# Performance work log

Hardware: AMD Instinct MI355X
Metric: run time of the kernel (lower is better)

## Reference

```python
import jax, jax.numpy as jnp
import numpy as np

B, K, N = 32768, 8, 64
TN = 3 * N


def _P():
    # 9x9 vec-transpose permutation (matches the hand-built P in the torch module)
    P = np.zeros((9, 9), dtype=np.float32)
    rows = [0, 1, 2, 3, 4, 5, 6, 7, 8]
    cols = [0, 3, 6, 1, 4, 7, 2, 5, 8]
    P[rows, cols] = 1.0
    return jnp.asarray(P)


def _precompute(b, w, lam):
    # b: (K,3,N), w: (1,N,1), lam: scalar
    wsum = jnp.sum(w)
    b_w = (b @ w)[..., 0] / wsum                       # (K,3)
    sw = jnp.sqrt(w).reshape(1, 1, N)                  # (1,1,N)
    bar_b = sw * (b - b_w[:, :, None])                 # (K,3,N)
    bar_B = bar_b.transpose(0, 2, 1).reshape(K, TN).T  # (3N,K)
    bar_H = 2.0 * (bar_B.T @ bar_B + lam * jnp.eye(K, dtype=b.dtype))
    Hinv = jnp.linalg.inv(bar_H)
    Htemp = Hinv @ jnp.ones((K, 1), dtype=b.dtype)     # (K,1)
    s = jnp.sum(Htemp)
    G = Hinv - (Htemp @ Htemp.T) / s                   # (K,K)
    g = Htemp / s                                      # (K,1)
    M = jnp.concatenate([
        2.0 * bar_B @ (G @ bar_B.T) - jnp.eye(TN, dtype=b.dtype),  # (3N,3N)
        2.0 * jnp.sqrt(lam) * (G @ bar_B.T),                        # (K,3N)
    ], axis=0)                                         # (3N+K,3N)
    h = jnp.concatenate([bar_B @ g, jnp.sqrt(lam) * g], axis=0)  # (3N+K,1)
    return bar_B, G, g, M, h, b_w, wsum


def setup_inputs() -> dict:
    key = jax.random.key(0)
    k1, k2 = jax.random.split(key)
    y = jax.random.normal(k1, (B, 3, N), dtype=jnp.float32)
    b = jax.random.normal(k2, (K, 3, N), dtype=jnp.float32)
    w = jnp.ones((1, N, 1), dtype=jnp.float32)
    lam = jnp.ones((1,), dtype=jnp.float32)
    return {"y": y, "b": b, "w": w, "lam": lam}


def reference(y, b, w, lam):
    lam = jnp.squeeze(lam)
    Pm = _P()
    bar_B, G, g, M, h, b_w, wsum = _precompute(b, w, lam)

    # weighted centroid + centered/weighted keypoints
    y_w = (y @ w) / wsum                               # (B,3,1)
    sw = jnp.sqrt(w).reshape(1, 1, N)
    bar_y = sw * (y - y_w)                             # (B,3,N)

    # Batched Q build. kron(Y^T, I3) contraction done implicitly:
    # (M @ kron(Y^T,I3))[a, 3m+j] = sum_n M[a,3n+j] * Y[m,n]
    M_r = M.reshape(TN + K, N, 3)                      # (A,N,3)
    E = jnp.einsum('anj,bmn->bamj', M_r, bar_y).reshape(B, TN + K, 9) @ Pm  # tempE: (B,A,9)
    q_top = jnp.einsum('a,bae->be', h[:, 0], E)        # Q[0,1:]: (B,9)
    Q00 = jnp.sum(h * h)
    Q_low = jnp.einsum('bae,baf->bef', E, E)           # Q[1:,1:]: (B,9,9)

    Q = jnp.zeros((B, 10, 10), dtype=y.dtype)
    Q = Q.at[:, 0, 0].set(Q00)
    Q = Q.at[:, 0, 1:].set(q_top)
    Q = Q.at[:, 1:, 0].set(q_top)
    Q = Q.at[:, 1:, 1:].set(Q_low)

    # Tight SDP relaxation solution: X* = v v^T with v the eigenvector of Q
    # at the smallest eigenvalue; the original then takes top eigvec of X,
    # which recovers the same v.
    ev, evec = jnp.linalg.eigh(Q)
    vec = evec[:, :, 0]                                # smallest-eigenvalue eigvec, (B,10)
    vec = vec / vec[:, :1]
    R = vec[:, 1:].reshape(B, 3, 3).transpose(0, 2, 1)  # (B,3,3)

    # shape coefficients: c = 2 * G bar_B^T kron(I_N, R^T) vec(bar_y^T) + g
    A = G @ bar_B.T                                    # (K,3N)
    Bv = jnp.einsum('bji,bjn->bni', R, bar_y).reshape(B, TN, 1)
    c = 2.0 * (A @ Bv) + g                             # (B,K,1)

    # translation
    t = y_w - R @ (b_w.T @ c)                          # (B,3,1)
    return R, t, c
```

## Files before the change

### kernel.cpp

```cpp
#include <hip/hip_runtime.h>
#include <math.h>

static constexpr int Bn = 32768;

#define WS_G     1792
#define WS_g     1856
#define WS_BW    1864
#define WS_Q00   1888
#define WS_WSUM  1889
#define WS_CB4   2048

__host__ __device__ constexpr int tidx(int i, int j) { return i*10 - i*(i+1)/2 + j; }
__host__ __device__ constexpr int lidx(int i, int j) { return i*(i+1)/2 + j; }

__global__ void k_pre(const float* __restrict__ bb, const float* __restrict__ w,
                      const float* __restrict__ lam, float* __restrict__ ws)
{
  __shared__ float s_w[64], s_sw[64], s_bw[24], s_barb[64][24];
  __shared__ float s_BtB[64];
  __shared__ float s_M[8][16];
  __shared__ float s_u[8], s_g[8], s_red[64], s_wsum, s_s;
  const int t = threadIdx.x;
  const int i8 = t >> 3, j8 = t & 7;
  const float lv = lam[0];

  s_w[t]  = w[t];
  s_sw[t] = sqrtf(fmaxf(s_w[t], 0.0f));
  __syncthreads();
  if (t == 0) { float a = 0; for (int n = 0; n < 64; n++) a += s_w[n]; s_wsum = a; }
  __syncthreads();
  const float wsum = s_wsum;
  if (t < 24) {
    float a = 0;
    for (int n = 0; n < 64; n++) a += bb[t*64 + n] * s_w[n];
    s_bw[t] = a / wsum;
  }
  __syncthreads();
  for (int km = 0; km < 24; ++km)
    s_barb[t][km] = s_sw[t] * (bb[km*64 + t] - s_bw[km]);
  __syncthreads();
  {
    float a = 0;
    for (int n = 0; n < 64; n++)
      for (int j = 0; j < 3; j++)
        a += s_barb[n][i8*3 + j] * s_barb[n][j8*3 + j];
    s_BtB[t] = a;
  }
  __syncthreads();
  s_M[i8][j8]     = 2.0f * (s_BtB[t] + ((i8 == j8) ? lv : 0.0f));
  s_M[i8][8 + j8] = (i8 == j8) ? 1.0f : 0.0f;
#pragma unroll
  for (int k = 0; k < 8; k++) {
    __syncthreads();
    const float fk  = s_M[i8][k];
    const float piv = 1.0f / s_M[k][k];
    __syncthreads();
    if (i8 == k) { s_M[k][j8] *= piv; s_M[k][8 + j8] *= piv; }
    __syncthreads();
    if (i8 != k) {
      s_M[i8][j8]     -= fk * s_M[k][j8];
      s_M[i8][8 + j8] -= fk * s_M[k][8 + j8];
    }
  }
  __syncthreads();
  if (t < 8) {
    float a = 0;
#pragma unroll
    for (int j = 0; j < 8; j++) a += s_M[t][8 + j];
    s_u[t] = a;
  }
  __syncthreads();
  if (t == 0) {
    float s = 0;
#pragma unroll
    for (int j = 0; j < 8; j++) s += s_u[j];
    s_s = s;
  }
  __syncthreads();
  const float s = s_s;
  if (t < 8) s_g[t] = s_u[t] / s;
  const float Gel = s_M[i8][8 + j8] - s_u[i8] * s_u[j8] / s;
  ws[WS_G + t] = Gel;
  __syncthreads();
  s_red[t] = s_g[i8] * (s_BtB[t] + ((i8 == j8) ? lv : 0.0f)) * s_g[j8];
  __syncthreads();
  if (t == 0) {
    float a = 0;
    for (int n = 0; n < 64; n++) a += s_red[n];
    ws[WS_Q00]  = a;
    ws[WS_WSUM] = wsum;
  }
  if (t < 8)  ws[WS_g + t]  = s_g[t];
  if (t < 24) ws[WS_BW + t] = s_bw[t];
  {
    float* p = ws + WS_CB4 + (t >> 4)*520 + (t & 15)*32;
    p[0] = s_w[t]; p[1] = 0; p[2] = 0; p[3] = 0;
#pragma unroll
    for (int km = 0; km < 24; km++)
      p[4 + km] = s_sw[t] * s_barb[t][km];
#pragma unroll
    for (int i = 28; i < 32; i++) p[i] = 0;
  }
}

__global__ __launch_bounds__(256, 2) void k_main(const float* __restrict__ y,
                                                 const float* __restrict__ ws,
                                                 float* __restrict__ out)
{
  __shared__ float s_cb[4*520];
  __shared__ float s_G[64], s_g8[8], s_bw[24];
  __shared__ float s_Q[55][66];
  const int t   = threadIdx.x;
  const int lb  = t >> 2;
  const int sub = t & 3;
  const int b   = blockIdx.x * 64 + lb;

  for (int i = t; i < 4*520; i += 256) s_cb[i] = ws[WS_CB4 + i];
  if (t < 64) s_G[t]  = ws[WS_G + t];
  if (t < 8)  s_g8[t] = ws[WS_g + t];
  if (t >= 8 && t < 32) s_bw[t - 8] = ws[WS_BW + (t - 8)];
  const float q00v = ws[WS_Q00];
  const float wsum = ws[WS_WSUM];
  __syncthreads();

  const float* yb = y + (size_t)b * 192;
  float F[24][3];
  float gw[6];
  float ywa[3] = {0, 0, 0};
#pragma unroll
  for (int i = 0; i < 24; i++) { F[i][0] = 0; F[i][1] = 0; F[i][2] = 0; }
#pragma unroll
  for (int i = 0; i < 6; i++) gw[i] = 0;

  const float* plane = s_cb + sub*520;
#pragma unroll
  for (int i4 = 0; i4 < 4; i4++) {
    const int n4 = sub*4 + i4;
    float4 v0 = reinterpret_cast<const float4*>(yb)[n4];
    float4 v1 = reinterpret_cast<const float4*>(yb + 64)[n4];
    float4 v2 = reinterpret_cast<const float4*>(yb + 128)[n4];
    float a0[4] = {v0.x, v0.y, v0.z, v0.w};
    float a1[4] = {v1.x, v1.y, v1.z, v1.w};
    float a2[4] = {v2.x, v2.y, v2.z, v2.w};
#pragma unroll
    for (int l = 0; l < 4; l++) {
      const int ni = 4*i4 + l;
      const float4* row = reinterpret_cast<const float4*>(plane + ni*32);
      float4 c0 = row[0];
      float4 ch[6];
#pragma unroll
      for (int cc = 0; cc < 6; cc++) ch[cc] = row[1 + cc];
      const float cb[24] = {ch[0].x, ch[0].y, ch[0].z, ch[0].w,
                            ch[1].x, ch[1].y, ch[1].z, ch[1].w,
                            ch[2].x, ch[2].y, ch[2].z, ch[2].w,
                            ch[3].x, ch[3].y, ch[3].z, ch[3].w,
                            ch[4].x, ch[4].y, ch[4].z, ch[4].w,
                            ch[5].x, ch[5].y, ch[5].z, ch[5].w};
      float ym0 = a0[l], ym1 = a1[l], ym2 = a2[l];
      float wn  = c0.x;
      float wy0 = wn*ym0, wy1 = wn*ym1, wy2 = wn*ym2;
      ywa[0] += wy0; ywa[1] += wy1; ywa[2] += wy2;
      gw[0] += wy0*ym0; gw[1] += wy0*ym1; gw[2] += wy0*ym2;
      gw[3] += wy1*ym1; gw[4] += wy1*ym2; gw[5] += wy2*ym2;
#pragma unroll
      for (int km = 0; km < 24; km++) {
        F[km][0] += cb[km]*ym0; F[km][1] += cb[km]*ym1; F[km][2] += cb[km]*ym2;
      }
    }
  }
#pragma unroll
  for (int km = 0; km < 24; km++)
#pragma unroll
    for (int m = 0; m < 3; m++) {
      float v = F[km][m];
      v += __shfl_xor(v, 1);
      v += __shfl_xor(v, 2);
      F[km][m] = v;
    }
#pragma unroll
  for (int i = 0; i < 6; i++) { float v = gw[i]; v += __shfl_xor(v, 1); v += __shfl_xor(v, 2); gw[i] = v; }
#pragma unroll
  for (int i = 0; i < 3; i++) { float v = ywa[i]; v += __shfl_xor(v, 1); v += __shfl_xor(v, 2); ywa[i] = v; }

  const float iws = 1.0f / wsum;
  float yw[3] = {ywa[0]*iws, ywa[1]*iws, ywa[2]*iws};
  float Gram[6];
  Gram[0] = gw[0] - ywa[0]*ywa[0]*iws;
  Gram[1] = gw[1] - ywa[0]*ywa[1]*iws;
  Gram[2] = gw[2] - ywa[0]*ywa[2]*iws;
  Gram[3] = gw[3] - ywa[1]*ywa[1]*iws;
  Gram[4] = gw[4] - ywa[1]*ywa[2]*iws;
  Gram[5] = gw[5] - ywa[2]*ywa[2]*iws;

  if (sub == 0) s_Q[0][lb] = q00v;
#pragma unroll
  for (int e = 0; e < 9; e++) {
    const int j = e / 3, m = e % 3;
    float a = 0;
#pragma unroll
    for (int k = 0; k < 8; k++) a += s_g8[k] * F[k*3 + j][m];
    if ((e & 3) == sub) s_Q[tidx(0, 1 + e)][lb] = -a;
  }
  float F6[6][3];
#pragma unroll
  for (int kk = 0; kk < 6; kk++)
#pragma unroll
    for (int m = 0; m < 3; m++) {
      float x01 = (sub & 1) ? F[6 + kk][m]  : F[kk][m];
      float x23 = (sub & 1) ? F[18 + kk][m] : F[12 + kk][m];
      F6[kk][m] = (sub & 2) ? x23 : x01;
    }
  float FGr[2][9];
#pragma unroll
  for (int kk = 0; kk < 2; kk++) {
    float gcol[8];
#pragma unroll
    for (int k = 0; k < 8; k++) {
      float g01 = (sub & 1) ? s_G[k*8 + 2 + kk] : s_G[k*8 + 0 + kk];
      float g23 = (sub & 1) ? s_G[k*8 + 6 + kk] : s_G[k*8 + 4 + kk];
      gcol[k] = (sub & 2) ? g23 : g01;
    }
#pragma unroll
    for (int e = 0; e < 9; e++) {
      const int j = e / 3, m = e % 3;
      float a = 0;
#pragma unroll
      for (int k = 0; k < 8; k++) a += gcol[k] * F[k*3 + j][m];
      FGr[kk][e] = a;
    }
  }
#pragma unroll
  for (int e = 0; e < 9; e++)
#pragma unroll
    for (int f = e; f < 9; f++) {
      const int j = e/3, m = e%3, j2 = f/3, m2 = f%3;
      float p = FGr[0][e] * F6[j2][m2] + FGr[1][e] * F6[3 + j2][m2];
      p += __shfl_xor(p, 1);
      p += __shfl_xor(p, 2);
      if ((tidx(1 + e, 1 + f) & 3) == sub) {
        const float gterm = (j == j2) ? Gram[(m <= m2) ? (m*3 - m*(m+1)/2 + m2) : (m2*3 - m2*(m2+1)/2 + m)] : 0.0f;
        s_Q[tidx(1 + e, 1 + f)][lb] = -2.0f*p + gterm;
      }
    }
  __syncthreads();

  float Mm[55];
#pragma unroll
  for (int i = 0; i < 10; i++)
#pragma unroll
    for (int j = 0; j <= i; j++)
      Mm[lidx(i,j)] = s_Q[tidx(j,i)][lb];

  float ad[10], b2[9];
#pragma unroll
  for (int j = 0; j < 8; j++) {
    float s2 = 0;
#pragma unroll
    for (int i = j + 1; i < 10; i++) s2 += Mm[lidx(i,j)] * Mm[lidx(i,j)];
    const float x0 = Mm[lidx(j+1,j)];
    const float anorm = __builtin_amdgcn_sqrtf(s2);
    const float alpha = (x0 > 0.0f) ? -anorm : anorm;
    const float uu = s2 - alpha * x0;
    const float beta = (uu > 1e-35f) ? __builtin_amdgcn_rcpf(uu) : 0.0f;
    float u[10], p[10];
    u[j+1] = x0 - alpha;
#pragma unroll
    for (int i = j + 2; i < 10; i++) u[i] = Mm[lidx(i,j)];
#pragma unroll
    for (int i = j + 1; i < 10; i++) {
      float acc = 0;
#pragma unroll
      for (int k = j + 1; k < 10; k++) acc += Mm[(i >= k) ? lidx(i,k) : lidx(k,i)] * u[k];
      p[i] = beta * acc;
    }
    float K = 0;
#pragma unroll
    for (int i = j + 1; i < 10; i++) K += u[i] * p[i];
    K *= 0.5f * beta;
#pragma unroll
    for (int i = j + 1; i < 10; i++) p[i] -= K * u[i];
#pragma unroll
    for (int i = j + 1; i < 10; i++)
#pragma unroll
      for (int k = j + 1; k <= i; k++)
        Mm[lidx(i,k)] -= u[i]*p[k] + p[i]*u[k];
    ad[j] = Mm[lidx(j,j)];
    b2[j] = s2;
  }
  ad[8] = Mm[lidx(8,8)];
  ad[9] = Mm[lidx(9,9)];
  b2[8] = Mm[lidx(9,8)] * Mm[lidx(9,8)];

  float b2max = b2[0];
#pragma unroll
  for (int i = 1; i < 9; i++) b2max = fmaxf(b2max, b2[i]);
  const float pm = 1e-20f * b2max + 1e-30f;

  float lo = 0.0f, hi = s_Q[0][lb];
#pragma unroll
  for (int j = 1; j < 10; j++) hi = fminf(hi, s_Q[tidx(j,j)][lb]);

  const int base = (t & 63) & ~3;
  const float subf = (sub == 0) ? 2.0f : (float)sub;
  for (int round = 0; round < 11; ++round) {
    const float quart = 0.25f * (hi - lo);
    const float mid = lo + quart * subf;
    int neg = 0;
    float d = ad[0] - mid;
    neg += (d < 0.0f) ? 1 : 0;
#pragma unroll
    for (int i = 1; i < 10; i++) {
      d = (fabsf(d) < pm) ? -pm : d;
      d = ad[i] - mid - b2[i-1] * __builtin_amdgcn_rcpf(d);
      neg += (d < 0.0f) ? 1 : 0;
    }
    const int n1 = __shfl(neg, base | 1);
    const int n2 = __shfl(neg, base | 2);
    const int n3 = __shfl(neg, base | 3);
    const float m1 = lo + quart, m2v = lo + 2.0f*quart, m3 = lo + 3.0f*quart;
    const float nlo = (n3 == 0) ? m3 : (n2 == 0) ? m2v : (n1 == 0) ? m1 : lo;
    const float nhi = (n1 > 0) ? m1 : (n2 > 0) ? m2v : (n3 > 0) ? m3 : hi;
    lo = nlo; hi = nhi;
  }

  float M[55], id[10];
#pragma unroll
  for (int i = 0; i < 10; i++)
#pragma unroll
    for (int j = 0; j <= i; j++)
      M[lidx(i,j)] = s_Q[tidx(j,i)][lb];
  float tr = 0.0f;
#pragma unroll
  for (int i = 0; i < 10; i++) tr += M[lidx(i,i)];
  const float delta = 1e-5f * fabsf(tr) + 1e-30f;
  const float sigma = lo - delta;
#pragma unroll
  for (int i = 0; i < 10; i++) M[lidx(i,i)] -= sigma;

#pragma unroll
  for (int j = 0; j < 10; j++) {
    float d = M[lidx(j,j)];
#pragma unroll
    for (int t2 = 0; t2 < j; t2++) d -= M[lidx(j,t2)] * M[lidx(j,t2)];
    d = fmaxf(d, 1e-30f);
    float is = __builtin_amdgcn_rsqf(d);
    id[j] = is;
#pragma unroll
    for (int i = j + 1; i < 10; i++) {
      float a = M[lidx(i,j)];
#pragma unroll
      for (int t2 = 0; t2 < j; t2++) a -= M[lidx(i,t2)] * M[lidx(j,t2)];
      M[lidx(i,j)] = a * is;
    }
  }

  float x[10];
#pragma unroll
  for (int i = 0; i < 10; i++) x[i] = 1.0f;
#pragma unroll
  for (int it = 0; it < 3; ++it) {
#pragma unroll
    for (int i = 0; i < 10; i++) {
      float a = x[i];
#pragma unroll
      for (int j = 0; j < i; j++) a -= M[lidx(i,j)] * x[j];
      x[i] = a * id[i];
    }
#pragma unroll
    for (int i = 9; i >= 0; i--) {
      float a = x[i];
#pragma unroll
      for (int j = i + 1; j < 10; j++) a -= M[lidx(j,i)] * x[j];
      x[i] = a * id[i];
    }
    float s2 = 0;
#pragma unroll
    for (int i = 0; i < 10; i++) s2 += x[i]*x[i];
    float sc = __builtin_amdgcn_rsqf(s2 + 1e-38f);
#pragma unroll
    for (int i = 0; i < 10; i++) x[i] *= sc;
  }

  const float inv0 = __builtin_amdgcn_rcpf(x[0]);
  float R[3][3];
#pragma unroll
  for (int r = 0; r < 3; r++)
#pragma unroll
    for (int cc = 0; cc < 3; cc++)
      R[r][cc] = x[1 + 3*cc + r] * inv0;

  float cv[2];
#pragma unroll
  for (int kk = 0; kk < 2; kk++) {
    const int k = sub*2 + kk;
    float a = 0;
#pragma unroll
    for (int e = 0; e < 9; e++) a += x[1 + e] * FGr[kk][e];
    cv[kk] = 2.0f * inv0 * a + s_g8[k];
    out[(size_t)12*Bn + (size_t)b*8 + k] = cv[kk];
  }
  float um0 = s_bw[(sub*2)*3 + 0]*cv[0] + s_bw[(sub*2 + 1)*3 + 0]*cv[1];
  float um1 = s_bw[(sub*2)*3 + 1]*cv[0] + s_bw[(sub*2 + 1)*3 + 1]*cv[1];
  float um2 = s_bw[(sub*2)*3 + 2]*cv[0] + s_bw[(sub*2 + 1)*3 + 2]*cv[1];
  um0 += __shfl_xor(um0, 1); um0 += __shfl_xor(um0, 2);
  um1 += __shfl_xor(um1, 1); um1 += __shfl_xor(um1, 2);
  um2 += __shfl_xor(um2, 1); um2 += __shfl_xor(um2, 2);

#pragma unroll
  for (int r = 0; r < 3; r++)
#pragma unroll
    for (int cc = 0; cc < 3; cc++)
      if (((r*3 + cc) & 3) == sub)
        out[(size_t)b*9 + r*3 + cc] = R[r][cc];
  if (sub == 0) {
#pragma unroll
    for (int r = 0; r < 3; r++)
      out[(size_t)9*Bn + (size_t)b*3 + r] = yw[r] - (R[r][0]*um0 + R[r][1]*um1 + R[r][2]*um2);
  }
}

extern "C" void kernel_launch(void* const* d_in, const int* in_sizes, int n_in,
                              void* d_out, int out_size, void* d_ws, size_t ws_size,
                              hipStream_t stream) {
  const float* y   = (const float*)d_in[0];
  const float* bb  = (const float*)d_in[1];
  const float* w   = (const float*)d_in[2];
  const float* lam = (const float*)d_in[3];
  float* ws  = (float*)d_ws;
  float* out = (float*)d_out;
  k_pre <<<1,      64, 0, stream>>>(bb, w, lam, ws);
  k_main<<<Bn/64, 256, 0, stream>>>(y, ws, out);
}
```

Baseline: 42.59 us.

## Fuse precompute kernel into main kernel, recomputing constants per block

The single-block precompute kernel is removed. Every block of the main kernel now redundantly computes the centroid, bar_B, the 8x8 inverse, G, g and Q00 in shared memory using its first 64 threads, then proceeds as before. This removes a kernel launch, the serial dependency and the workspace round trip. In exchange each of the 512 blocks repeats a small serial Gauss-Jordan and reductions behind several barriers, and shared memory use per block grows, which may limit occupancy.

```diff
diff --git a/kernel.cpp b/kernel.cpp
--- a/kernel.cpp
+++ b/kernel.cpp
@@ -3,29 +3,33 @@
 
 static constexpr int Bn = 32768;
 
-#define WS_G     1792
-#define WS_g     1856
-#define WS_BW    1864
-#define WS_Q00   1888
-#define WS_WSUM  1889
-#define WS_CB4   2048
-
 __host__ __device__ constexpr int tidx(int i, int j) { return i*10 - i*(i+1)/2 + j; }
 __host__ __device__ constexpr int lidx(int i, int j) { return i*(i+1)/2 + j; }
 
-__global__ void k_pre(const float* __restrict__ bb, const float* __restrict__ w,
-                      const float* __restrict__ lam, float* __restrict__ ws)
+__global__ __launch_bounds__(256, 2) void k_main(const float* __restrict__ y,
+                                                 const float* __restrict__ bb,
+                                                 const float* __restrict__ w,
+                                                 const float* __restrict__ lam,
+                                                 float* __restrict__ out)
 {
-  __shared__ float s_w[64], s_sw[64], s_bw[24], s_barb[64][24];
+  __shared__ float s_w[64], s_sw[64], s_barb[64][24];
   __shared__ float s_BtB[64];
   __shared__ float s_M[8][16];
-  __shared__ float s_u[8], s_g[8], s_red[64], s_wsum, s_s;
-  const int t = threadIdx.x;
-  const int i8 = t >> 3, j8 = t & 7;
+  __shared__ float s_u[8], s_red[64];
+  __shared__ float s_wsum, s_q00;
+  __shared__ float s_cb[4*520];
+  __shared__ float s_G[64], s_g8[8], s_bw[24];
+  __shared__ float s_Q[55][66];
+
+  const int t   = threadIdx.x;
+  const bool act = (t < 64);
+  const int i8 = (t & 63) >> 3, j8 = t & 7;
   const float lv = lam[0];
 
-  s_w[t]  = w[t];
-  s_sw[t] = sqrtf(fmaxf(s_w[t], 0.0f));
+  if (act) {
+    s_w[t]  = w[t];
+    s_sw[t] = sqrtf(fmaxf(w[t], 0.0f));
+  }
   __syncthreads();
   if (t == 0) { float a = 0; for (int n = 0; n < 64; n++) a += s_w[n]; s_wsum = a; }
   __syncthreads();
@@ -36,10 +40,11 @@
     s_bw[t] = a / wsum;
   }
   __syncthreads();
-  for (int km = 0; km < 24; ++km)
-    s_barb[t][km] = s_sw[t] * (bb[km*64 + t] - s_bw[km]);
-  __syncthreads();
-  {
+  if (act)
+    for (int km = 0; km < 24; ++km)
+      s_barb[t][km] = s_sw[t] * (bb[km*64 + t] - s_bw[km]);
+  __syncthreads();
+  if (act) {
     float a = 0;
     for (int n = 0; n < 64; n++)
       for (int j = 0; j < 3; j++)
@@ -47,17 +52,19 @@
     s_BtB[t] = a;
   }
   __syncthreads();
-  s_M[i8][j8]     = 2.0f * (s_BtB[t] + ((i8 == j8) ? lv : 0.0f));
-  s_M[i8][8 + j8] = (i8 == j8) ? 1.0f : 0.0f;
+  if (act) {
+    s_M[i8][j8]     = 2.0f * (s_BtB[t] + ((i8 == j8) ? lv : 0.0f));
+    s_M[i8][8 + j8] = (i8 == j8) ? 1.0f : 0.0f;
+  }
 #pragma unroll
   for (int k = 0; k < 8; k++) {
     __syncthreads();
-    const float fk  = s_M[i8][k];
-    const float piv = 1.0f / s_M[k][k];
+    float fk = 0.0f, piv = 1.0f;
+    if (act) { fk = s_M[i8][k]; piv = 1.0f / s_M[k][k]; }
     __syncthreads();
-    if (i8 == k) { s_M[k][j8] *= piv; s_M[k][8 + j8] *= piv; }
+    if (act && i8 == k) { s_M[k][j8] *= piv; s_M[k][8 + j8] *= piv; }
     __syncthreads();
-    if (i8 != k) {
+    if (act && i8 != k) {
       s_M[i8][j8]     -= fk * s_M[k][j8];
       s_M[i8][8 + j8] -= fk * s_M[k][8 + j8];
     }
@@ -74,26 +81,24 @@
     float s = 0;
 #pragma unroll
     for (int j = 0; j < 8; j++) s += s_u[j];
-    s_s = s;
-  }
-  __syncthreads();
-  const float s = s_s;
-  if (t < 8) s_g[t] = s_u[t] / s;
-  const float Gel = s_M[i8][8 + j8] - s_u[i8] * s_u[j8] / s;
-  ws[WS_G + t] = Gel;
-  __syncthreads();
-  s_red[t] = s_g[i8] * (s_BtB[t] + ((i8 == j8) ? lv : 0.0f)) * s_g[j8];
+    s_red[0] = s;
+  }
+  __syncthreads();
+  {
+    const float s = s_red[0];
+    if (t < 8) s_g8[t] = s_u[t] / s;
+    if (act) s_G[t] = s_M[i8][8 + j8] - s_u[i8] * s_u[j8] / s;
+  }
+  __syncthreads();
+  if (act) s_red[t] = s_g8[i8] * (s_BtB[t] + ((i8 == j8) ? lv : 0.0f)) * s_g8[j8];
   __syncthreads();
   if (t == 0) {
     float a = 0;
     for (int n = 0; n < 64; n++) a += s_red[n];
-    ws[WS_Q00]  = a;
-    ws[WS_WSUM] = wsum;
-  }
-  if (t < 8)  ws[WS_g + t]  = s_g[t];
-  if (t < 24) ws[WS_BW + t] = s_bw[t];
-  {
-    float* p = ws + WS_CB4 + (t >> 4)*520 + (t & 15)*32;
+    s_q00 = a;
+  }
+  if (act) {
+    float* p = s_cb + (t >> 4)*520 + (t & 15)*32;
     p[0] = s_w[t]; p[1] = 0; p[2] = 0; p[3] = 0;
 #pragma unroll
     for (int km = 0; km < 24; km++)
@@ -101,28 +106,12 @@
 #pragma unroll
     for (int i = 28; i < 32; i++) p[i] = 0;
   }
-}
-
-__global__ __launch_bounds__(256, 2) void k_main(const float* __restrict__ y,
-                                                 const float* __restrict__ ws,
-                                                 float* __restrict__ out)
-{
-  __shared__ float s_cb[4*520];
-  __shared__ float s_G[64], s_g8[8], s_bw[24];
-  __shared__ float s_Q[55][66];
-  const int t   = threadIdx.x;
+  __syncthreads();
+  const float q00v = s_q00;
+
   const int lb  = t >> 2;
   const int sub = t & 3;
   const int b   = blockIdx.x * 64 + lb;
-
-  for (int i = t; i < 4*520; i += 256) s_cb[i] = ws[WS_CB4 + i];
-  if (t < 64) s_G[t]  = ws[WS_G + t];
-  if (t < 8)  s_g8[t] = ws[WS_g + t];
-  if (t >= 8 && t < 32) s_bw[t - 8] = ws[WS_BW + (t - 8)];
-  const float q00v = ws[WS_Q00];
-  const float wsum = ws[WS_WSUM];
-  __syncthreads();
-
   const float* yb = y + (size_t)b * 192;
   float F[24][3];
   float gw[6];
@@ -426,8 +415,7 @@
   const float* bb  = (const float*)d_in[1];
   const float* w   = (const float*)d_in[2];
   const float* lam = (const float*)d_in[3];
-  float* ws  = (float*)d_ws;
   float* out = (float*)d_out;
-  k_pre <<<1,      64, 0, stream>>>(bb, w, lam, ws);
-  k_main<<<Bn/64, 256, 0, stream>>>(y, ws, out);
+  (void)d_ws; (void)ws_size;
+  k_main<<<Bn/64, 256, 0, stream>>>(y, bb, w, lam, out);
 }
```

Measured after the change: 38.50 us. -9.6%, faster.
